# Kernel optimization log

Measured on AMD Instinct MI355X. Metric: run time of the kernel, lower is better.

Reference implementation:

```python
import jax, jax.numpy as jnp
import numpy as np
import math

NO, NR, E = 100000, 1000, 1000000
DO, DR, DE, H, OM = 64, 32, 4, 64, 32


def setup_inputs() -> dict:
    key = jax.random.key(0)
    ks = jax.random.split(key, 20)
    s = lambda k, sh: jax.random.normal(k, sh, dtype=jnp.float32) * 0.05
    inp = {
        'x_order': jax.random.normal(ks[0], (NO, DO), dtype=jnp.float32),
        'x_rider': jax.random.normal(ks[1], (NR, DR), dtype=jnp.float32),
        'edge_attr': jax.random.normal(ks[2], (E, DE), dtype=jnp.float32),
        'order_idx': jax.random.randint(ks[3], (E,), 0, NO),
        'rider_idx': jax.random.randint(ks[4], (E,), 0, NR),
        'omega_encoded': jax.random.normal(ks[5], (OM,), dtype=jnp.float32),
        # TransformerConv params (heads=1)
        'Wk': s(ks[6], (DO, H)), 'bk': jnp.zeros((H,), jnp.float32),
        'Wq': s(ks[7], (DR, H)), 'bq': jnp.zeros((H,), jnp.float32),
        'Wv': s(ks[8], (DO, H)), 'bv': jnp.zeros((H,), jnp.float32),
        'We': s(ks[9], (DE, H)),  # lin_edge, bias=False in PyG
        'Wskip': s(ks[10], (DR, H)), 'bskip': jnp.zeros((H,), jnp.float32),
        # order_proj
        'Wp': s(ks[11], (DO, H)), 'bp': jnp.zeros((H,), jnp.float32),
        # residual MLP: Linear(2H+OM,128) -> ReLU -> Linear(128,1)
        'W1': s(ks[12], (2 * H + OM, 128)), 'b1': jnp.zeros((128,), jnp.float32),
        'W2': s(ks[13], (128, 1)), 'b2': jnp.zeros((1,), jnp.float32),
    }
    return inp


def _segment_softmax(alpha, seg, num_segments):
    m = jax.ops.segment_max(alpha, seg, num_segments=num_segments)
    m = jnp.where(jnp.isfinite(m), m, 0.0)
    ex = jnp.exp(alpha - m[seg])
    denom = jax.ops.segment_sum(ex, seg, num_segments=num_segments)
    return ex / (denom[seg] + 1e-16)


def reference(x_order, x_rider, edge_attr, order_idx, rider_idx, omega_encoded,
              Wk, bk, Wq, bq, Wv, bv, We, Wskip, bskip, Wp, bp, W1, b1, W2, b2):
    scale = 1.0 / math.sqrt(H)
    # TransformerConv((order, rider) -> rider), heads=1, edge_dim
    q = x_rider @ Wq + bq            # [NR, H]
    k = x_order @ Wk + bk            # [NO, H]
    v = x_order @ Wv + bv            # [NO, H]
    e = edge_attr @ We               # [E, H]
    k_j = k[order_idx] + e           # [E, H]
    v_j = v[order_idx] + e           # [E, H]
    alpha = jnp.sum(q[rider_idx] * k_j, axis=-1) * scale  # [E]
    alpha = _segment_softmax(alpha, rider_idx, NR)
    agg = jax.ops.segment_sum(alpha[:, None] * v_j, rider_idx, num_segments=NR)  # [NR, H]
    rider_emb = agg + x_rider @ Wskip + bskip  # root/skip connection

    # edge scoring
    order_proj = x_order @ Wp + bp   # [NO, H]
    oe = order_proj[order_idx]       # [E, H]
    re = rider_emb[rider_idx]        # [E, H]
    dot = jnp.sum(oe * re, axis=-1) * scale  # [E]
    omega_expand = jnp.broadcast_to(omega_encoded[None, :], (oe.shape[0], OM))
    resid_in = jnp.concatenate([oe, re, omega_expand], axis=-1)  # [E, 2H+OM]
    hmid = jax.nn.relu(resid_in @ W1 + b1)
    resid = (hmid @ W2 + b2)[:, 0]
    return jnp.clip(dot + resid, -10.0, 10.0)
```

## Files before the change

kernel.cpp:

```cpp
#include <hip/hip_runtime.h>
#include <hip/hip_bf16.h>
#include <math.h>
#include <stdint.h>

#define NO_N 100000
#define NR_N 1000
#define E_N  1000000
#define SB     250
#define SCHUNK 4000
#define KVP_TILES 1563
#define KVP_BLKS 1024
#define MAXTILES 17008

typedef short bf16x8 __attribute__((ext_vector_type(8)));
typedef float floatx4 __attribute__((ext_vector_type(4)));

__device__ __forceinline__ unsigned short bfu(float x) {
    union { __hip_bfloat16 h; unsigned short u; } c;
    c.h = __float2bfloat16(x);
    return c.u;
}
__device__ __forceinline__ float bflo(unsigned int u) {
    return __uint_as_float(u << 16);
}
__device__ __forceinline__ float bfhi(unsigned int u) {
    return __uint_as_float(u & 0xffff0000u);
}

__global__ __launch_bounds__(256) void k_front(
    const float* __restrict__ xr,
    const float* __restrict__ Wq, const float* __restrict__ bq,
    const float* __restrict__ Wskip, const float* __restrict__ bskip,
    const float* __restrict__ We,
    float* __restrict__ q, float* __restrict__ skip, float* __restrict__ t,
    const float* __restrict__ W1, const float* __restrict__ b1,
    const float* __restrict__ omega, float* __restrict__ b1eff,
    unsigned short* __restrict__ w1t,
    const float* __restrict__ x,
    const float* __restrict__ Wk, const float* __restrict__ bk,
    const float* __restrict__ Wv, const float* __restrict__ bv,
    const float* __restrict__ Wp, const float* __restrict__ bp,
    unsigned short* __restrict__ kb, unsigned short* __restrict__ vb,
    unsigned short* __restrict__ pb,
    const int* __restrict__ ridx, int* __restrict__ ghist)
{
    __shared__ __align__(16) char smem[9216];
    const int tid = threadIdx.x;
    const int b = blockIdx.x;

    if (b < 250) {
        float* sx = (float*)smem;
        float* sq = sx + 128;
        int rbase = b * 4;
        if (tid < 128) {
            int rl = tid >> 5, d = tid & 31;
            sx[rl * 32 + d] = xr[(rbase + rl) * 32 + d];
        }
        __syncthreads();
        int rl = tid >> 6, h = tid & 63;
        int r = rbase + rl;
        float aq = bq[h], as = bskip[h];
        #pragma unroll 4
        for (int d = 0; d < 32; ++d) {
            float xv = sx[rl * 32 + d];
            aq += xv * Wq[d * 64 + h];
            as += xv * Wskip[d * 64 + h];
        }
        sq[rl * 64 + h] = aq;
        q[r * 64 + h] = aq;
        skip[r * 64 + h] = as;
        __syncthreads();
        if (tid < 16) {
            int rl2 = tid >> 2, d = tid & 3;
            float acc = 0.f;
            for (int hh = 0; hh < 64; ++hh)
                acc += We[d * 64 + hh] * sq[rl2 * 64 + hh];
            t[(rbase + rl2) * 4 + d] = acc;
        }
    } else if (b == 250) {
        if (tid < 128) {
            float acc = b1[tid];
            #pragma unroll 4
            for (int j = 0; j < 32; ++j)
                acc += omega[j] * W1[(128 + j) * 128 + tid];
            b1eff[tid] = acc;
        }
        for (int idx = tid; idx < 64 * 128; idx += 256) {
            int n = idx >> 6, k = idx & 63;
            w1t[idx] = bfu(W1[k * 128 + n]);
        }
    } else if (b < 251 + KVP_BLKS) {
        unsigned short* sX = (unsigned short*)smem;
        const int wave = tid >> 6, lane = tid & 63;
        const int l15 = lane & 15, quad = lane >> 4;

        bf16x8 bfr[3][2];
        float bias[3];
        unsigned short* outT[3];
        int colc[3];
        #pragma unroll
        for (int ct = 0; ct < 3; ++ct) {
            int n = wave * 48 + ct * 16 + l15;
            int table = n >> 6, c = n & 63;
            const float* W  = (table == 0) ? Wk : (table == 1) ? Wv : Wp;
            const float* bb = (table == 0) ? bk : (table == 1) ? bv : bp;
            bias[ct] = bb[c];
            colc[ct] = c;
            outT[ct] = (table == 0) ? kb : (table == 1) ? vb : pb;
            #pragma unroll
            for (int kf = 0; kf < 2; ++kf) {
                bf16x8 f;
                #pragma unroll
                for (int j = 0; j < 8; ++j)
                    f[j] = (short)bfu(W[(size_t)(kf * 32 + quad * 8 + j) * 64 + c]);
                bfr[ct][kf] = f;
            }
        }

        const int srl = tid >> 2;
        const int sqt = (tid & 3) * 16;

        for (int tile = b - 251; tile < KVP_TILES; tile += KVP_BLKS) {
            int rowbase = tile * 64;
            {
                int row = rowbase + srl;
                unsigned short* dst = sX + srl * 72 + sqt;
                if (row < NO_N) {
                    const float4* src = (const float4*)(x + (size_t)row * 64 + sqt);
                    #pragma unroll
                    for (int i = 0; i < 4; ++i) {
                        float4 a = src[i];
                        ushort4 u = { bfu(a.x), bfu(a.y), bfu(a.z), bfu(a.w) };
                        *(ushort4*)(dst + i * 4) = u;
                    }
                } else {
                    ushort4 z = {0, 0, 0, 0};
                    #pragma unroll
                    for (int i = 0; i < 4; ++i) *(ushort4*)(dst + i * 4) = z;
                }
            }
            __syncthreads();

            floatx4 acc[4][3];
            #pragma unroll
            for (int rt = 0; rt < 4; ++rt)
                #pragma unroll
                for (int ct = 0; ct < 3; ++ct)
                    acc[rt][ct] = (floatx4){bias[ct], bias[ct], bias[ct], bias[ct]};

            #pragma unroll
            for (int rt = 0; rt < 4; ++rt) {
                const unsigned short* ar = sX + (size_t)(rt * 16 + l15) * 72 + quad * 8;
                bf16x8 a0 = *(const bf16x8*)(ar);
                bf16x8 a1 = *(const bf16x8*)(ar + 32);
                #pragma unroll
                for (int ct = 0; ct < 3; ++ct) {
                    floatx4 c = acc[rt][ct];
                    c = __builtin_amdgcn_mfma_f32_16x16x32_bf16(a0, bfr[ct][0], c, 0, 0, 0);
                    c = __builtin_amdgcn_mfma_f32_16x16x32_bf16(a1, bfr[ct][1], c, 0, 0, 0);
                    acc[rt][ct] = c;
                }
            }

            #pragma unroll
            for (int rt = 0; rt < 4; ++rt) {
                int rb = rowbase + rt * 16 + quad * 4;
                #pragma unroll
                for (int ct = 0; ct < 3; ++ct) {
                    unsigned short* o = outT[ct];
                    size_t cbase = colc[ct];
                    #pragma unroll
                    for (int g = 0; g < 4; ++g) {
                        int row = rb + g;
                        if (row < NO_N)
                            o[(size_t)row * 64 + cbase] = bfu(acc[rt][ct][g]);
                    }
                }
            }
            __syncthreads();
        }
    } else {
        int* hc = (int*)smem;
        int hb = b - (251 + KVP_BLKS);
        for (int i = tid; i < NR_N; i += 256) hc[i] = 0;
        __syncthreads();
        int s = hb * SCHUNK;
        for (int i = s + tid; i < s + SCHUNK; i += 256)
            atomicAdd(&hc[ridx[i]], 1);
        __syncthreads();
        for (int i = tid; i < NR_N; i += 256)
            ghist[i * SB + hb] = hc[i];
    }
}

__global__ __launch_bounds__(256) void k_colscan(const int* __restrict__ ghist,
                                                 int* __restrict__ gpre,
                                                 int* __restrict__ counts)
{
    __shared__ int s[256];
    int tid = threadIdx.x, r = blockIdx.x;
    int v = (tid < SB) ? ghist[r * SB + tid] : 0;
    s[tid] = v;
    __syncthreads();
    for (int off = 1; off < 256; off <<= 1) {
        int tv = (tid >= off) ? s[tid - off] : 0;
        __syncthreads();
        s[tid] += tv;
        __syncthreads();
    }
    if (tid < SB) gpre[r * SB + tid] = s[tid] - v;
    if (tid == 255) counts[r] = s[255];
}

__global__ __launch_bounds__(1024) void k_scan(const int* __restrict__ counts,
                                               int* __restrict__ offsets,
                                               int* __restrict__ tilestart)
{
    __shared__ int s[1024];
    int tid = threadIdx.x;
    int c = (tid < NR_N) ? counts[tid] : 0;
    s[tid] = c;
    __syncthreads();
    for (int off = 1; off < 1024; off <<= 1) {
        int tv = (tid >= off) ? s[tid - off] : 0;
        __syncthreads();
        s[tid] += tv;
        __syncthreads();
    }
    if (tid < NR_N) offsets[tid] = s[tid] - c;
    if (tid == NR_N - 1) offsets[NR_N] = s[tid];
    __syncthreads();
    int tc = (tid < NR_N) ? ((c + 63) >> 6) : 0;
    s[tid] = tc;
    __syncthreads();
    for (int off = 1; off < 1024; off <<= 1) {
        int tv = (tid >= off) ? s[tid - off] : 0;
        __syncthreads();
        s[tid] += tv;
        __syncthreads();
    }
    if (tid < NR_N) tilestart[tid] = s[tid] - tc;
    if (tid == NR_N - 1) tilestart[NR_N] = s[tid];
}

__global__ __launch_bounds__(256) void k_trec(const int* __restrict__ tilestart,
                                              const int* __restrict__ offsets,
                                              int4* __restrict__ trec)
{
    int nt = tilestart[NR_N];
    int t = blockIdx.x * 256 + threadIdx.x;
    if (t >= nt) return;
    int lo = 0, hi = NR_N - 1;
    while (lo < hi) {
        int mid = (lo + hi + 1) >> 1;
        if (tilestart[mid] <= t) lo = mid; else hi = mid - 1;
    }
    trec[t] = make_int4(lo, offsets[lo] + ((t - tilestart[lo]) << 6),
                        offsets[lo + 1], 0);
}

__global__ __launch_bounds__(1024) void k_scatter2(
    const int* __restrict__ ridx, const int* __restrict__ oidx,
    const float* __restrict__ ea, const float* __restrict__ t,
    const int* __restrict__ offsets, const int* __restrict__ gpre,
    int4* __restrict__ spack, int* __restrict__ so, int* __restrict__ rank)
{
    __shared__ int cur[NR_N];
    int tid = threadIdx.x, b = blockIdx.x;
    for (int i = tid; i < NR_N; i += 1024)
        cur[i] = offsets[i] + gpre[i * SB + b];
    __syncthreads();
    int s = b * SCHUNK;
    for (int i = s + tid; i < s + SCHUNK; i += 1024) {
        int r = ridx[i];
        int o = oidx[i];
        float4 e4 = *(const float4*)(ea + (size_t)i * 4);
        float4 t4 = *(const float4*)(t + r * 4);
        float h = e4.x * t4.x + e4.y * t4.y + e4.z * t4.z + e4.w * t4.w;
        int pos = atomicAdd(&cur[r], 1);
        int4 pk;
        pk.x = o;
        pk.y = __float_as_int(h);
        pk.z = (int)((unsigned)bfu(e4.x) | ((unsigned)bfu(e4.y) << 16));
        pk.w = (int)((unsigned)bfu(e4.z) | ((unsigned)bfu(e4.w) << 16));
        spack[pos] = pk;
        so[pos] = o;
        rank[i] = pos;
    }
}

__global__ __launch_bounds__(512) void k_rider(
    const int* __restrict__ offsets, const int4* __restrict__ spack,
    const float* __restrict__ q,
    const unsigned short* __restrict__ kb, const unsigned short* __restrict__ vb,
    const float* __restrict__ We, const float* __restrict__ skip,
    const float* __restrict__ W1, const float* __restrict__ b1eff,
    unsigned short* __restrict__ embb, float* __restrict__ Br)
{
    __shared__ float sQ[64];
    __shared__ int2 sOX[8][64];
    __shared__ float rv[8][64];
    __shared__ float re4[8][4];
    __shared__ float rd[8];

    int r = blockIdx.x;
    int wave = threadIdx.x >> 6, lane = threadIdx.x & 63;
    if (threadIdx.x < 64) sQ[threadIdx.x] = q[r * 64 + threadIdx.x];
    __syncthreads();

    int beg = offsets[r], end = offsets[r + 1];
    int cnt = end - beg;
    int chunk = (cnt + 7) >> 3;
    int s0 = beg + wave * chunk;
    int s1 = min(s0 + chunk, end);

    float aggv = 0.f, dsum = 0.f;
    float ag0 = 0.f, ag1 = 0.f, ag2 = 0.f, ag3 = 0.f;
    const float2* sQ2 = (const float2*)sQ;

    for (int jb = s0; jb < s1; jb += 64) {
        int j = jb + lane;
        bool valid = (j < s1);
        int4 pk = make_int4(0, 0, 0, 0);
        if (valid) pk = spack[j];
        int oo = pk.x;
        float h = __int_as_float(pk.y);

        const uint4* krow = (const uint4*)(kb + (size_t)oo * 64);
        uint4 K0 = krow[0], K1 = krow[1], K2 = krow[2], K3 = krow[3];
        uint4 K4 = krow[4], K5 = krow[5], K6 = krow[6], K7 = krow[7];
        float acc = h;
        #define DOT8(Kv, base) { \
            float2 qa = sQ2[(base) + 0]; \
            acc = fmaf(bflo(Kv.x), qa.x, acc); acc = fmaf(bfhi(Kv.x), qa.y, acc); \
            float2 qb = sQ2[(base) + 1]; \
            acc = fmaf(bflo(Kv.y), qb.x, acc); acc = fmaf(bfhi(Kv.y), qb.y, acc); \
            float2 qc = sQ2[(base) + 2]; \
            acc = fmaf(bflo(Kv.z), qc.x, acc); acc = fmaf(bfhi(Kv.z), qc.y, acc); \
            float2 qd = sQ2[(base) + 3]; \
            acc = fmaf(bflo(Kv.w), qd.x, acc); acc = fmaf(bfhi(Kv.w), qd.y, acc); }
        DOT8(K0, 0) DOT8(K1, 4) DOT8(K2, 8) DOT8(K3, 12)
        DOT8(K4, 16) DOT8(K5, 20) DOT8(K6, 24) DOT8(K7, 28)
        #undef DOT8

        float exv = valid ? __expf(acc * 0.125f) : 0.f;
        dsum += exv;
        unsigned int ez = (unsigned int)pk.z, ew = (unsigned int)pk.w;
        ag0 = fmaf(exv, bflo(ez), ag0);
        ag1 = fmaf(exv, bfhi(ez), ag1);
        ag2 = fmaf(exv, bflo(ew), ag2);
        ag3 = fmaf(exv, bfhi(ew), ag3);

        sOX[wave][lane] = make_int2(oo, __float_as_int(exv));

        int nn = min(s1 - jb, 64);
        int i = 0;
        for (; i + 8 <= nn; i += 8) {
            int2 x0 = sOX[wave][i + 0], x1 = sOX[wave][i + 1];
            int2 x2 = sOX[wave][i + 2], x3 = sOX[wave][i + 3];
            int2 x4 = sOX[wave][i + 4], x5 = sOX[wave][i + 5];
            int2 x6 = sOX[wave][i + 6], x7 = sOX[wave][i + 7];
            unsigned short u0 = vb[(size_t)x0.x * 64 + lane];
            unsigned short u1 = vb[(size_t)x1.x * 64 + lane];
            unsigned short u2 = vb[(size_t)x2.x * 64 + lane];
            unsigned short u3 = vb[(size_t)x3.x * 64 + lane];
            unsigned short u4 = vb[(size_t)x4.x * 64 + lane];
            unsigned short u5 = vb[(size_t)x5.x * 64 + lane];
            unsigned short u6 = vb[(size_t)x6.x * 64 + lane];
            unsigned short u7 = vb[(size_t)x7.x * 64 + lane];
            aggv = fmaf(__int_as_float(x0.y), __uint_as_float((unsigned int)u0 << 16), aggv);
            aggv = fmaf(__int_as_float(x1.y), __uint_as_float((unsigned int)u1 << 16), aggv);
            aggv = fmaf(__int_as_float(x2.y), __uint_as_float((unsigned int)u2 << 16), aggv);
            aggv = fmaf(__int_as_float(x3.y), __uint_as_float((unsigned int)u3 << 16), aggv);
            aggv = fmaf(__int_as_float(x4.y), __uint_as_float((unsigned int)u4 << 16), aggv);
            aggv = fmaf(__int_as_float(x5.y), __uint_as_float((unsigned int)u5 << 16), aggv);
            aggv = fmaf(__int_as_float(x6.y), __uint_as_float((unsigned int)u6 << 16), aggv);
            aggv = fmaf(__int_as_float(x7.y), __uint_as_float((unsigned int)u7 << 16), aggv);
        }
        for (; i < nn; ++i) {
            int2 xx = sOX[wave][i];
            unsigned short uu = vb[(size_t)xx.x * 64 + lane];
            aggv = fmaf(__int_as_float(xx.y), __uint_as_float((unsigned int)uu << 16), aggv);
        }
    }

    #pragma unroll
    for (int m = 1; m < 64; m <<= 1) {
        dsum += __shfl_xor(dsum, m);
        ag0 += __shfl_xor(ag0, m);
        ag1 += __shfl_xor(ag1, m);
        ag2 += __shfl_xor(ag2, m);
        ag3 += __shfl_xor(ag3, m);
    }

    rv[wave][lane] = aggv;
    if (lane == 0) {
        rd[wave] = dsum;
        re4[wave][0] = ag0; re4[wave][1] = ag1;
        re4[wave][2] = ag2; re4[wave][3] = ag3;
    }
    __syncthreads();
    if (threadIdx.x < 64) {
        int l = threadIdx.x;
        float av = 0.f, ds = 0.f, a0 = 0.f, a1 = 0.f, a2 = 0.f, a3 = 0.f;
        #pragma unroll
        for (int w = 0; w < 8; ++w) {
            av += rv[w][l]; ds += rd[w];
            a0 += re4[w][0]; a1 += re4[w][1]; a2 += re4[w][2]; a3 += re4[w][3];
        }
        float corr = a0 * We[0 * 64 + l] + a1 * We[1 * 64 + l]
                   + a2 * We[2 * 64 + l] + a3 * We[3 * 64 + l];
        float val = (av + corr) / (ds + 1e-16f) + skip[r * 64 + l];
        embb[r * 64 + l] = bfu(val);
        sQ[l] = val;
    }
    __syncthreads();
    if (threadIdx.x < 128) {
        int c = threadIdx.x;
        float a = b1eff[c];
        #pragma unroll 8
        for (int d = 0; d < 64; ++d)
            a = fmaf(sQ[d], W1[(size_t)(64 + d) * 128 + c], a);
        Br[r * 128 + c] = a;
    }
}

__global__ __launch_bounds__(256) void k_edge2(
    const int* __restrict__ so, const int4* __restrict__ trec,
    const int* __restrict__ tilestart,
    const unsigned short* __restrict__ pb, const unsigned short* __restrict__ embb,
    const float* __restrict__ Br, const unsigned short* __restrict__ w1t,
    const float* __restrict__ W2, const float* __restrict__ b2,
    float* __restrict__ tmp)
{
    const int tid = threadIdx.x;
    const int wave = tid >> 6;
    const int lane = tid & 63;
    const int l15 = lane & 15;
    const int quad = lane >> 4;

    bf16x8 bfr[8][2];
    float w2v[8];
    #pragma unroll
    for (int ctl = 0; ctl < 8; ++ctl) {
        int n = ctl * 16 + l15;
        w2v[ctl] = W2[n];
        bfr[ctl][0] = *(const bf16x8*)(w1t + n * 64 + quad * 8);
        bfr[ctl][1] = *(const bf16x8*)(w1t + n * 64 + 32 + quad * 8);
    }
    float b2v = b2[0];
    const int ntiles = tilestart[NR_N];
    const bf16x8 z8 = (bf16x8){0, 0, 0, 0, 0, 0, 0, 0};

    union U4B { uint4 u; bf16x8 b; };

    for (int tile = blockIdx.x * 4 + wave; tile < ntiles; tile += gridDim.x * 4) {
        int4 rr = trec[tile];
        const int r = rr.x, jb = rr.y, jend = rr.z;

        int o_l = so[min(jb + lane, jend - 1)];
        U4B A0[4], A1[4];
        #pragma unroll
        for (int rt = 0; rt < 4; ++rt) {
            int osrc = __shfl(o_l, rt * 16 + l15);
            const unsigned short* rowp = pb + (size_t)osrc * 64 + quad * 8;
            A0[rt].u = *(const uint4*)(rowp);
            A1[rt].u = *(const uint4*)(rowp + 32);
        }

        const unsigned short* eb = embb + r * 64;
        bf16x8 e0 = *(const bf16x8*)(eb + quad * 8);
        bf16x8 e1 = *(const bf16x8*)(eb + 32 + quad * 8);
        bf16x8 b80 = z8, b81 = z8;
        if (l15 == 0) { b80 = e0; b81 = e1; }

        float brv[8];
        #pragma unroll
        for (int ctl = 0; ctl < 8; ++ctl)
            brv[ctl] = Br[r * 128 + ctl * 16 + l15];

        #pragma unroll
        for (int rt = 0; rt < 4; ++rt) {
            floatx4 s = (floatx4){0.f, 0.f, 0.f, 0.f};
            #pragma unroll
            for (int ctl = 0; ctl < 8; ++ctl) {
                floatx4 c = (floatx4){brv[ctl], brv[ctl], brv[ctl], brv[ctl]};
                c = __builtin_amdgcn_mfma_f32_16x16x32_bf16(A0[rt].b, bfr[ctl][0], c, 0, 0, 0);
                c = __builtin_amdgcn_mfma_f32_16x16x32_bf16(A1[rt].b, bfr[ctl][1], c, 0, 0, 0);
                #pragma unroll
                for (int g = 0; g < 4; ++g)
                    s[g] = fmaf(fmaxf(c[g], 0.f), w2v[ctl], s[g]);
            }
            floatx4 c8 = (floatx4){0.f, 0.f, 0.f, 0.f};
            c8 = __builtin_amdgcn_mfma_f32_16x16x32_bf16(A0[rt].b, b80, c8, 0, 0, 0);
            c8 = __builtin_amdgcn_mfma_f32_16x16x32_bf16(A1[rt].b, b81, c8, 0, 0, 0);

            #pragma unroll
            for (int m = 1; m < 16; m <<= 1) {
                s[0] += __shfl_xor(s[0], m);
                s[1] += __shfl_xor(s[1], m);
                s[2] += __shfl_xor(s[2], m);
                s[3] += __shfl_xor(s[3], m);
            }
            if (l15 == 0) {
                int rowb = rt * 16 + quad * 4;
                #pragma unroll
                for (int g = 0; g < 4; ++g) {
                    int pos = jb + rowb + g;
                    if (pos < jend) {
                        float v = s[g] + 0.125f * c8[g] + b2v;
                        tmp[pos] = fminf(fmaxf(v, -10.f), 10.f);
                    }
                }
            }
        }
    }
}

__global__ __launch_bounds__(256) void k_perm(const int* __restrict__ rank,
                                              const float* __restrict__ tmp,
                                              float* __restrict__ out)
{
    int i = blockIdx.x * 256 + threadIdx.x;
    if (i < E_N) out[i] = tmp[rank[i]];
}

extern "C" void kernel_launch(void* const* d_in, const int* in_sizes, int n_in,
                              void* d_out, int out_size, void* d_ws, size_t ws_size,
                              hipStream_t stream)
{
    const float* x_order   = (const float*)d_in[0];
    const float* x_rider   = (const float*)d_in[1];
    const float* edge_attr = (const float*)d_in[2];
    const int*   order_idx = (const int*)d_in[3];
    const int*   rider_idx = (const int*)d_in[4];
    const float* omega     = (const float*)d_in[5];
    const float* Wk = (const float*)d_in[6];  const float* bk = (const float*)d_in[7];
    const float* Wq = (const float*)d_in[8];  const float* bq = (const float*)d_in[9];
    const float* Wv = (const float*)d_in[10]; const float* bv = (const float*)d_in[11];
    const float* We = (const float*)d_in[12];
    const float* Wskip = (const float*)d_in[13]; const float* bskip = (const float*)d_in[14];
    const float* Wp = (const float*)d_in[15]; const float* bp = (const float*)d_in[16];
    const float* W1 = (const float*)d_in[17]; const float* b1 = (const float*)d_in[18];
    const float* W2 = (const float*)d_in[19]; const float* b2 = (const float*)d_in[20];
    float* out = (float*)d_out;

    unsigned short* ws_kb = (unsigned short*)d_ws;
    unsigned short* ws_vb = ws_kb + (size_t)NO_N * 64;
    unsigned short* ws_pb = ws_vb + (size_t)NO_N * 64;
    int4* ws_spack = (int4*)(ws_pb + (size_t)NO_N * 64);
    float* ws_tmp  = (float*)ws_spack;
    int*  ws_so    = (int*)(ws_spack + E_N);
    int*  ws_rank  = ws_so + E_N;
    float* wsf     = (float*)(ws_rank + E_N);
    float* ws_q    = wsf;
    float* ws_skip = ws_q + NR_N * 64;
    unsigned short* ws_embb = (unsigned short*)(ws_skip + NR_N * 64);
    float* ws_t    = (float*)(ws_embb + NR_N * 64);
    float* ws_b1e  = ws_t + NR_N * 4;
    unsigned short* ws_w1t = (unsigned short*)(ws_b1e + 128);
    float* ws_Br   = (float*)(ws_w1t + 128 * 64);
    int* ws_counts  = (int*)(ws_Br + NR_N * 128);
    int* ws_offsets = ws_counts + NR_N;
    int* ws_tilest  = ws_offsets + NR_N + 8;
    int* ws_ghist   = ws_tilest + NR_N + 8;
    int* ws_gpre    = ws_ghist + NR_N * SB;
    int4* ws_trec   = (int4*)(((uintptr_t)(ws_gpre + NR_N * SB) + 15) & ~(uintptr_t)15);

    k_front<<<251 + KVP_BLKS + SB, 256, 0, stream>>>(
        x_rider, Wq, bq, Wskip, bskip, We, ws_q, ws_skip, ws_t,
        W1, b1, omega, ws_b1e, ws_w1t,
        x_order, Wk, bk, Wv, bv, Wp, bp, ws_kb, ws_vb, ws_pb,
        rider_idx, ws_ghist);
    k_colscan<<<NR_N, 256, 0, stream>>>(ws_ghist, ws_gpre, ws_counts);
    k_scan<<<1, 1024, 0, stream>>>(ws_counts, ws_offsets, ws_tilest);
    k_trec<<<(MAXTILES + 255) / 256, 256, 0, stream>>>(ws_tilest, ws_offsets, ws_trec);
    k_scatter2<<<SB, 1024, 0, stream>>>(rider_idx, order_idx, edge_attr, ws_t,
                                        ws_offsets, ws_gpre, ws_spack, ws_so, ws_rank);
    k_rider<<<NR_N, 512, 0, stream>>>(ws_offsets, ws_spack, ws_q,
                                      ws_kb, ws_vb, We, ws_skip,
                                      W1, ws_b1e, ws_embb, ws_Br);
    k_edge2<<<1536, 256, 0, stream>>>(ws_so, ws_trec, ws_tilest,
                                      ws_pb, ws_embb, ws_Br, ws_w1t, W2, b2, ws_tmp);
    k_perm<<<(E_N + 255) / 256, 256, 0, stream>>>(ws_rank, ws_tmp, out);
}
```

Before: 293.0 us.

## Swap MFMA operands in edge MLP, prefetch next tile indices, shrink grid

The edge-scoring kernel swaps the A and B operands of the MFMA so each lane's output column maps to one edge. That replaces the 16-lane shuffle reduction with two cross-quad shuffles and lets a whole quad store results in one go. It also software-prefetches the next tile's record and order indices across loop iterations, and reads the Br bias directly as float4 per quad instead of broadcasting scalars. The grid drops from 1536 to 1024 blocks, trading some parallelism for longer-lived waves that benefit from the prefetch.

```diff
diff --git a/kernel.cpp b/kernel.cpp
--- a/kernel.cpp
+++ b/kernel.cpp
@@ -440,13 +440,13 @@
     const int quad = lane >> 4;
 
     bf16x8 bfr[8][2];
-    float w2v[8];
+    floatx4 w2q[8];
     #pragma unroll
     for (int ctl = 0; ctl < 8; ++ctl) {
         int n = ctl * 16 + l15;
-        w2v[ctl] = W2[n];
         bfr[ctl][0] = *(const bf16x8*)(w1t + n * 64 + quad * 8);
         bfr[ctl][1] = *(const bf16x8*)(w1t + n * 64 + 32 + quad * 8);
+        w2q[ctl] = *(const floatx4*)(W2 + ctl * 16 + quad * 4);
     }
     float b2v = b2[0];
     const int ntiles = tilestart[NR_N];
@@ -454,66 +454,73 @@
 
     union U4B { uint4 u; bf16x8 b; };
 
-    for (int tile = blockIdx.x * 4 + wave; tile < ntiles; tile += gridDim.x * 4) {
-        int4 rr = trec[tile];
+    const int stride = gridDim.x * 4;
+    int tile = blockIdx.x * 4 + wave;
+    if (tile >= ntiles) return;
+
+    int4 rr = trec[tile];
+    int o_rt[4];
+    #pragma unroll
+    for (int rt = 0; rt < 4; ++rt)
+        o_rt[rt] = so[min(rr.y + rt * 16 + l15, rr.z - 1)];
+
+    for (; tile < ntiles; tile += stride) {
         const int r = rr.x, jb = rr.y, jend = rr.z;
 
-        int o_l = so[min(jb + lane, jend - 1)];
         U4B A0[4], A1[4];
         #pragma unroll
         for (int rt = 0; rt < 4; ++rt) {
-            int osrc = __shfl(o_l, rt * 16 + l15);
-            const unsigned short* rowp = pb + (size_t)osrc * 64 + quad * 8;
+            const unsigned short* rowp = pb + (size_t)o_rt[rt] * 64 + quad * 8;
             A0[rt].u = *(const uint4*)(rowp);
             A1[rt].u = *(const uint4*)(rowp + 32);
         }
 
+        int4 rrn = trec[min(tile + stride, ntiles - 1)];
+        int o_nx[4];
+        #pragma unroll
+        for (int rt = 0; rt < 4; ++rt)
+            o_nx[rt] = so[min(rrn.y + rt * 16 + l15, rrn.z - 1)];
+
         const unsigned short* eb = embb + r * 64;
-        bf16x8 e0 = *(const bf16x8*)(eb + quad * 8);
-        bf16x8 e1 = *(const bf16x8*)(eb + 32 + quad * 8);
         bf16x8 b80 = z8, b81 = z8;
-        if (l15 == 0) { b80 = e0; b81 = e1; }
-
-        float brv[8];
-        #pragma unroll
-        for (int ctl = 0; ctl < 8; ++ctl)
-            brv[ctl] = Br[r * 128 + ctl * 16 + l15];
+        if (l15 == 0) {
+            b80 = *(const bf16x8*)(eb + quad * 8);
+            b81 = *(const bf16x8*)(eb + 32 + quad * 8);
+        }
+
+        const float* brrow = Br + r * 128;
 
         #pragma unroll
         for (int rt = 0; rt < 4; ++rt) {
-            floatx4 s = (floatx4){0.f, 0.f, 0.f, 0.f};
+            float s = 0.f;
             #pragma unroll
             for (int ctl = 0; ctl < 8; ++ctl) {
-                floatx4 c = (floatx4){brv[ctl], brv[ctl], brv[ctl], brv[ctl]};
-                c = __builtin_amdgcn_mfma_f32_16x16x32_bf16(A0[rt].b, bfr[ctl][0], c, 0, 0, 0);
-                c = __builtin_amdgcn_mfma_f32_16x16x32_bf16(A1[rt].b, bfr[ctl][1], c, 0, 0, 0);
+                floatx4 c = *(const floatx4*)(brrow + ctl * 16 + quad * 4);
+                c = __builtin_amdgcn_mfma_f32_16x16x32_bf16(bfr[ctl][0], A0[rt].b, c, 0, 0, 0);
+                c = __builtin_amdgcn_mfma_f32_16x16x32_bf16(bfr[ctl][1], A1[rt].b, c, 0, 0, 0);
                 #pragma unroll
                 for (int g = 0; g < 4; ++g)
-                    s[g] = fmaf(fmaxf(c[g], 0.f), w2v[ctl], s[g]);
+                    s = fmaf(fmaxf(c[g], 0.f), w2q[ctl][g], s);
             }
             floatx4 c8 = (floatx4){0.f, 0.f, 0.f, 0.f};
-            c8 = __builtin_amdgcn_mfma_f32_16x16x32_bf16(A0[rt].b, b80, c8, 0, 0, 0);
-            c8 = __builtin_amdgcn_mfma_f32_16x16x32_bf16(A1[rt].b, b81, c8, 0, 0, 0);
-
-            #pragma unroll
-            for (int m = 1; m < 16; m <<= 1) {
-                s[0] += __shfl_xor(s[0], m);
-                s[1] += __shfl_xor(s[1], m);
-                s[2] += __shfl_xor(s[2], m);
-                s[3] += __shfl_xor(s[3], m);
-            }
-            if (l15 == 0) {
-                int rowb = rt * 16 + quad * 4;
-                #pragma unroll
-                for (int g = 0; g < 4; ++g) {
-                    int pos = jb + rowb + g;
-                    if (pos < jend) {
-                        float v = s[g] + 0.125f * c8[g] + b2v;
-                        tmp[pos] = fminf(fmaxf(v, -10.f), 10.f);
-                    }
+            c8 = __builtin_amdgcn_mfma_f32_16x16x32_bf16(b80, A0[rt].b, c8, 0, 0, 0);
+            c8 = __builtin_amdgcn_mfma_f32_16x16x32_bf16(b81, A1[rt].b, c8, 0, 0, 0);
+
+            s += __shfl_xor(s, 16);
+            s += __shfl_xor(s, 32);
+
+            if (quad == 0) {
+                int pos = jb + rt * 16 + l15;
+                if (pos < jend) {
+                    float v = s + 0.125f * c8[0] + b2v;
+                    tmp[pos] = fminf(fmaxf(v, -10.f), 10.f);
                 }
             }
         }
+
+        rr = rrn;
+        #pragma unroll
+        for (int rt = 0; rt < 4; ++rt) o_rt[rt] = o_nx[rt];
     }
 }
 
@@ -580,7 +587,7 @@
     k_rider<<<NR_N, 512, 0, stream>>>(ws_offsets, ws_spack, ws_q,
                                       ws_kb, ws_vb, We, ws_skip,
                                       W1, ws_b1e, ws_embb, ws_Br);
-    k_edge2<<<1536, 256, 0, stream>>>(ws_so, ws_trec, ws_tilest,
+    k_edge2<<<1024, 256, 0, stream>>>(ws_so, ws_trec, ws_tilest,
                                       ws_pb, ws_embb, ws_Br, ws_w1t, W2, b2, ws_tmp);
     k_perm<<<(E_N + 255) / 256, 256, 0, stream>>>(ws_rank, ws_tmp, out);
 }
```

Result: faster. 281.7 us (-3.8%).
